# Kernel optimization log

Hardware: AMD Instinct MI355X
Metric: run time of the kernel (lower is better)

Reference implementation:

```python
import jax, jax.numpy as jnp
import numpy as np

N_NODES = 100000
N_EDGES = 3200000
F_IN = 128
HID = 256
EMB = 128
N_GRAPHS = 2048
N_CLASSES = 2


def _glorot(key, fan_in, fan_out):
    scale = np.sqrt(2.0 / (fan_in + fan_out)).astype(np.float32)
    return jax.random.normal(key, (fan_in, fan_out), jnp.float32) * scale


def setup_inputs() -> dict:
    key = jax.random.key(0)
    ks = jax.random.split(key, 12)
    x = jax.random.normal(ks[0], (N_NODES, F_IN), jnp.float32)
    edge_index = jax.random.randint(ks[1], (2, N_EDGES), 0, N_NODES, dtype=jnp.int64)
    batch = jnp.sort(jax.random.randint(ks[2], (N_NODES,), 0, N_GRAPHS, dtype=jnp.int64))
    return {
        "x": x,
        "edge_index": edge_index,
        "batch": batch,
        # GCN layer weights (input->hid, hid->hid, hid->emb)
        "W1": _glorot(ks[3], F_IN, HID), "b1": jnp.zeros((HID,), jnp.float32),
        "W2": _glorot(ks[4], HID, HID), "b2": jnp.zeros((HID,), jnp.float32),
        "W3": _glorot(ks[5], HID, EMB), "b3": jnp.zeros((EMB,), jnp.float32),
        # MLP classifier head
        "Wc1": _glorot(ks[6], EMB, HID), "bc1": jnp.zeros((HID,), jnp.float32),
        "Wc2": _glorot(ks[7], HID, HID // 2), "bc2": jnp.zeros((HID // 2,), jnp.float32),
        "Wc3": _glorot(ks[8], HID // 2, N_CLASSES), "bc3": jnp.zeros((N_CLASSES,), jnp.float32),
    }


def _gcn_conv(x, W, b, src, dst, dinv):
    # GCNConv with self loops: out = D^{-1/2}(A+I)D^{-1/2} (x @ W) + b
    h = x @ W  # [N, out]
    norm_e = dinv[src] * dinv[dst]  # [E]
    msg = h[src] * norm_e[:, None]
    agg = jax.ops.segment_sum(msg, dst, num_segments=N_NODES)
    agg = agg + h * (dinv * dinv)[:, None]  # self-loop term
    return agg + b


def reference(x, edge_index, batch, W1, b1, W2, b2, W3, b3, Wc1, bc1, Wc2, bc2, Wc3, bc3):
    src, dst = edge_index[0], edge_index[1]
    # degree including self loop (shared across layers)
    deg = jax.ops.segment_sum(jnp.ones((N_EDGES,), x.dtype), dst, num_segments=N_NODES) + 1.0
    dinv = jax.lax.rsqrt(deg)

    h = jax.nn.relu(_gcn_conv(x, W1, b1, src, dst, dinv))
    h = jax.nn.relu(_gcn_conv(h, W2, b2, src, dst, dinv))
    h = _gcn_conv(h, W3, b3, src, dst, dinv)  # final layer: no activation

    # mean pooling per graph
    sums = jax.ops.segment_sum(h, batch, num_segments=N_GRAPHS)  # [G, EMB]
    counts = jax.ops.segment_sum(jnp.ones((N_NODES,), h.dtype), batch, num_segments=N_GRAPHS)
    pooled = sums / jnp.maximum(counts, 1.0)[:, None]

    # MLP head (dropout is identity at eval)
    z = jax.nn.relu(pooled @ Wc1 + bc1)
    z = jax.nn.relu(z @ Wc2 + bc2)
    logits = z @ Wc3 + bc3  # [G, num_classes]
    return logits
```

## Files before the change

### kernel.cpp

```cpp
#include <hip/hip_runtime.h>
#include <cstdint>
#include <cstddef>

#define NODES  100000
#define EDGES  3200000
#define FIN    128
#define HIDDEN 256
#define EMBD   128
#define GRAPHS 2048

#define NB   256
#define NPB  391
#define CAP  16384
#define TILE 4096

typedef _Float16 f16;
typedef f16 f16x2 __attribute__((ext_vector_type(2)));
typedef f16 f16x4 __attribute__((ext_vector_type(4)));
typedef f16 f16x8 __attribute__((ext_vector_type(8)));
typedef float f32x4 __attribute__((ext_vector_type(4)));
typedef unsigned int u32;

__global__ __launch_bounds__(256) void binA_k(const int* __restrict__ src,
                                              const int* __restrict__ dst,
                                              u32* __restrict__ staging,
                                              int* __restrict__ gcur) {
  __shared__ u32 buf[TILE];
  __shared__ int bcnt[NB], bsh[NB], bstart[NB], bcur[NB], gbase[NB];
  const int tid = threadIdx.x;
  const int tb = blockIdx.x * TILE;

  bcnt[tid] = 0;
  __syncthreads();

#pragma unroll
  for (int j = 0; j < TILE / 256; ++j) {
    int i = tb + j * 256 + tid;
    if (i < EDGES) atomicAdd(&bcnt[dst[i] / NPB], 1);
  }
  __syncthreads();

  bsh[tid] = bcnt[tid];
  __syncthreads();
  for (int off = 1; off < NB; off <<= 1) {
    int t = (tid >= off) ? bsh[tid - off] : 0;
    __syncthreads();
    bsh[tid] += t;
    __syncthreads();
  }
  bstart[tid] = bsh[tid] - bcnt[tid];
  bcur[tid] = bsh[tid] - bcnt[tid];
  __syncthreads();

#pragma unroll
  for (int j = 0; j < TILE / 256; ++j) {
    int i = tb + j * 256 + tid;
    if (i < EDGES) {
      int d = dst[i];
      int b = d / NPB;
      u32 w = ((u32)src[i] << 9) | (u32)(d - b * NPB);
      buf[atomicAdd(&bcur[b], 1)] = w;
    }
  }
  gbase[tid] = atomicAdd(&gcur[tid], bcnt[tid]);
  __syncthreads();

  {
    int c = bcnt[tid], st = bstart[tid];
    u32* outp = staging + (size_t)tid * CAP + gbase[tid];
    for (int k = 0; k < c; ++k) outp[k] = buf[st + k];
  }
}

__global__ void bscan_k(const int* __restrict__ gcur, int* __restrict__ bbase) {
  __shared__ int sh[NB];
  int tid = threadIdx.x;
  int v = gcur[tid];
  sh[tid] = v;
  __syncthreads();
  for (int off = 1; off < NB; off <<= 1) {
    int t = (tid >= off) ? sh[tid - off] : 0;
    __syncthreads();
    sh[tid] += t;
    __syncthreads();
  }
  bbase[tid] = sh[tid] - v;
}

__global__ __launch_bounds__(512) void binB_k(const u32* __restrict__ staging,
                                              const int* __restrict__ gcur,
                                              const int* __restrict__ bbase,
                                              int* __restrict__ row_ptr,
                                              float* __restrict__ dinv,
                                              int* __restrict__ csr_src) {
  __shared__ int ncnt[512];
  __shared__ int ncur[512];
  const int b = blockIdx.x;
  const int tid = threadIdx.x;
  const int m = gcur[b];
  const int base = bbase[b];
  const int nb0 = b * NPB;
  const int nn = min(NPB, NODES - nb0);
  const u32* sb = staging + (size_t)b * CAP;

  ncnt[tid] = 0;
  __syncthreads();

  for (int k = tid; k < m; k += 512) atomicAdd(&ncnt[sb[k] & 511], 1);
  __syncthreads();

  int v = ncnt[tid];
  for (int off = 1; off < 512; off <<= 1) {
    int t = (tid >= off) ? ncnt[tid - off] : 0;
    __syncthreads();
    ncnt[tid] += t;
    __syncthreads();
  }
  int incl = ncnt[tid];
  if (tid < nn) {
    row_ptr[nb0 + tid + 1] = base + incl;
    dinv[nb0 + tid] = rsqrtf((float)(v + 1));
    ncur[tid] = base + incl - v;
  }
  if (b == 0 && tid == 0) row_ptr[0] = 0;
  __syncthreads();

  for (int k = tid; k < m; k += 512) {
    u32 w = sb[k];
    int pos = atomicAdd(&ncur[w & 511], 1);
    csr_src[pos] = (int)(w >> 9);
  }
}

__global__ void prescale_k(const float* __restrict__ x, const float* __restrict__ dinv,
                           f16* __restrict__ xs) {
  int idx = blockIdx.x * blockDim.x + threadIdx.x;
  if (idx >= NODES * FIN / 4) return;
  int row = idx >> 5;
  float4 v = *(const float4*)(x + (size_t)idx * 4);
  float d = dinv[row];
  f16x4 o = {(f16)(d * v.x), (f16)(d * v.y), (f16)(d * v.z), (f16)(d * v.w)};
  *(f16x4*)(xs + (size_t)idx * 4) = o;
}

__global__ void convw3_k(const float* __restrict__ W1, const float* __restrict__ W2,
                         const float* __restrict__ W3, f16* __restrict__ Wt1,
                         f16* __restrict__ Wt2, f16* __restrict__ Wt3) {
  int i = blockIdx.x * blockDim.x + threadIdx.x;
  if (i < 32768) {
    int k = i >> 8, m = i & 255;
    Wt1[(size_t)m * FIN + k] = (f16)W1[i];
  } else if (i < 98304) {
    int j = i - 32768;
    int k = j >> 8, m = j & 255;
    Wt2[(size_t)m * HIDDEN + k] = (f16)W2[j];
  } else if (i < 131072) {
    int j = i - 98304;
    int k = j >> 7, m = j & 127;
    Wt3[(size_t)m * HIDDEN + k] = (f16)W3[j];
  }
}

template <int V, bool FINAL>
__global__ __launch_bounds__(256) void agg_h(const f16* __restrict__ in, void* __restrict__ outv,
                      const int* __restrict__ row_ptr, const int* __restrict__ csr_src,
                      const float* __restrict__ dinv, const float* __restrict__ bias) {
  constexpr int D = V * 32;
  constexpr int U = 8;
  const int wid = (blockIdx.x * blockDim.x + threadIdx.x) >> 6;
  const int half = (threadIdx.x >> 5) & 1;
  const int lane = threadIdx.x & 31;
  const int node = wid * 2 + half;
  if (node >= NODES) return;
  const int c0 = lane * V;
  const f16* __restrict__ inc = in + c0;

  float acc[V];
#pragma unroll
  for (int v = 0; v < V; ++v) acc[v] = 0.f;

  const int beg = row_ptr[node], end = row_ptr[node + 1];
  int k = beg;
  if constexpr (V == 8) {
    for (; k + U <= end; k += U) {
      int s[U];
#pragma unroll
      for (int u = 0; u < U; ++u) s[u] = csr_src[k + u];
      f16x8 hv[U];
#pragma unroll
      for (int u = 0; u < U; ++u) hv[u] = *(const f16x8*)(inc + (size_t)s[u] * D);
#pragma unroll
      for (int u = 0; u < U; ++u)
#pragma unroll
        for (int v = 0; v < V; ++v) acc[v] += (float)hv[u][v];
    }
    for (; k < end; ++k) {
      f16x8 hv = *(const f16x8*)(inc + (size_t)csr_src[k] * D);
#pragma unroll
      for (int v = 0; v < V; ++v) acc[v] += (float)hv[v];
    }
    f16x8 hv = *(const f16x8*)(inc + (size_t)node * D);
#pragma unroll
    for (int v = 0; v < V; ++v) acc[v] += (float)hv[v];
  } else {
    for (; k + U <= end; k += U) {
      int s[U];
#pragma unroll
      for (int u = 0; u < U; ++u) s[u] = csr_src[k + u];
      f16x4 hv[U];
#pragma unroll
      for (int u = 0; u < U; ++u) hv[u] = *(const f16x4*)(inc + (size_t)s[u] * D);
#pragma unroll
      for (int u = 0; u < U; ++u)
#pragma unroll
        for (int v = 0; v < V; ++v) acc[v] += (float)hv[u][v];
    }
    for (; k < end; ++k) {
      f16x4 hv = *(const f16x4*)(inc + (size_t)csr_src[k] * D);
#pragma unroll
      for (int v = 0; v < V; ++v) acc[v] += (float)hv[v];
    }
    f16x4 hv = *(const f16x4*)(inc + (size_t)node * D);
#pragma unroll
    for (int v = 0; v < V; ++v) acc[v] += (float)hv[v];
  }

  const float di = dinv[node];
  if constexpr (FINAL) {
    float* out = (float*)outv;
    float4 o = {di * acc[0] + bias[c0], di * acc[1] + bias[c0 + 1],
                di * acc[2] + bias[c0 + 2], di * acc[3] + bias[c0 + 3]};
    *(float4*)(out + (size_t)node * D + c0) = o;
  } else {
    f16* out = (f16*)outv;
    if constexpr (V == 8) {
      f16x8 o;
#pragma unroll
      for (int v = 0; v < V; ++v) o[v] = (f16)(di * acc[v]);
      *(f16x8*)(out + (size_t)node * D + c0) = o;
    } else {
      f16x4 o;
#pragma unroll
      for (int v = 0; v < V; ++v) o[v] = (f16)(di * acc[v]);
      *(f16x4*)(out + (size_t)node * D + c0) = o;
    }
  }
}

template <int K>
__global__ __launch_bounds__(256, 2) void gemm_w(const f16* __restrict__ A,
                                                 const f16* __restrict__ Wt,
                                                 const float* __restrict__ bias,
                                                 const float* __restrict__ dinv,
                                                 f16* __restrict__ C, int N) {
  constexpr int M = 256;
  __shared__ f16 As[128][40];
  __shared__ f16 Bs[256][40];

  const int tid = threadIdx.x;
  const int rowbase = blockIdx.x * 128;
  const int l = tid & 63;
  const int wv = tid >> 6;
  const int wr = (wv >> 1) * 64;
  const int wc = (wv & 1) * 128;
  const int lr = tid >> 1;
  const int lc = (tid & 1) * 16;

  f32x4 acc[4][8];
#pragma unroll
  for (int i = 0; i < 4; ++i)
#pragma unroll
    for (int j = 0; j < 8; ++j) acc[i][j] = (f32x4){0.f, 0.f, 0.f, 0.f};

  const int arow = min(rowbase + lr, N - 1);
  const f16* aptr = A + (size_t)arow * K + lc;
  const f16* bptr = Wt + (size_t)tid * K;

  for (int kb = 0; kb < K; kb += 32) {
    *(f16x8*)&As[lr][lc]     = *(const f16x8*)(aptr + kb);
    *(f16x8*)&As[lr][lc + 8] = *(const f16x8*)(aptr + kb + 8);
#pragma unroll
    for (int q = 0; q < 4; ++q)
      *(f16x8*)&Bs[tid][q * 8] = *(const f16x8*)(bptr + kb + q * 8);
    __syncthreads();

    f16x8 a[4], b[8];
#pragma unroll
    for (int f = 0; f < 4; ++f)
      a[f] = *(const f16x8*)&As[wr + f * 16 + (l & 15)][(l >> 4) * 8];
#pragma unroll
    for (int g = 0; g < 8; ++g)
      b[g] = *(const f16x8*)&Bs[wc + g * 16 + (l & 15)][(l >> 4) * 8];
#pragma unroll
    for (int fm = 0; fm < 4; ++fm)
#pragma unroll
      for (int g = 0; g < 8; ++g)
        acc[fm][g] = __builtin_amdgcn_mfma_f32_16x16x32_f16(a[fm], b[g], acc[fm][g], 0, 0, 0);
    __syncthreads();
  }

  float bv[8];
#pragma unroll
  for (int g = 0; g < 8; ++g) bv[g] = bias[wc + g * 16 + (l & 15)];

#pragma unroll
  for (int fm = 0; fm < 4; ++fm) {
#pragma unroll
    for (int r = 0; r < 4; ++r) {
      int row = rowbase + wr + fm * 16 + (l >> 4) * 4 + r;
      if (row >= N) continue;
      float dv = dinv[row];
#pragma unroll
      for (int g = 0; g < 8; ++g) {
        int col = wc + g * 16 + (l & 15);
        float v = fmaxf(acc[fm][g][r] + bv[g], 0.f);
        C[(size_t)row * M + col] = (f16)(v * dv);
      }
    }
  }
}

template <int K, bool RELU, bool BIAS, bool DSCALE>
__global__ __launch_bounds__(256) void gemm_h(const f16* __restrict__ A,
                                              const f16* __restrict__ Wt,
                                              const float* __restrict__ bias,
                                              const float* __restrict__ dinv,
                                              f16* __restrict__ C, int N, int M) {
  __shared__ f16 As[128][40];
  __shared__ f16 Bs[128][40];

  const int tid = threadIdx.x;
  const int rowbase = blockIdx.x * 128;
  const int colbase = blockIdx.y * 128;
  const int l = tid & 63;
  const int wr = ((tid >> 6) >> 1) * 64;
  const int wc = ((tid >> 6) & 1) * 64;
  const int lr = tid >> 1;
  const int lc = (tid & 1) * 16;

  f32x4 acc[4][4];
#pragma unroll
  for (int i = 0; i < 4; ++i)
#pragma unroll
    for (int j = 0; j < 4; ++j) acc[i][j] = (f32x4){0.f, 0.f, 0.f, 0.f};

  const int arow = min(rowbase + lr, N - 1);
  const f16* aptr = A + (size_t)arow * K + lc;
  const f16* bptr = Wt + (size_t)(colbase + lr) * K + lc;

  for (int kb = 0; kb < K; kb += 32) {
    *(f16x8*)&As[lr][lc]     = *(const f16x8*)(aptr + kb);
    *(f16x8*)&As[lr][lc + 8] = *(const f16x8*)(aptr + kb + 8);
    *(f16x8*)&Bs[lr][lc]     = *(const f16x8*)(bptr + kb);
    *(f16x8*)&Bs[lr][lc + 8] = *(const f16x8*)(bptr + kb + 8);
    __syncthreads();

    f16x8 a[4], b[4];
#pragma unroll
    for (int f = 0; f < 4; ++f) {
      a[f] = *(const f16x8*)&As[wr + f * 16 + (l & 15)][(l >> 4) * 8];
      b[f] = *(const f16x8*)&Bs[wc + f * 16 + (l & 15)][(l >> 4) * 8];
    }
#pragma unroll
    for (int fm = 0; fm < 4; ++fm)
#pragma unroll
      for (int fn = 0; fn < 4; ++fn)
        acc[fm][fn] = __builtin_amdgcn_mfma_f32_16x16x32_f16(a[fm], b[fn], acc[fm][fn], 0, 0, 0);
    __syncthreads();
  }

  float bv[4];
#pragma unroll
  for (int fn = 0; fn < 4; ++fn)
    bv[fn] = BIAS ? bias[colbase + wc + fn * 16 + (l & 15)] : 0.f;

#pragma unroll
  for (int fm = 0; fm < 4; ++fm) {
#pragma unroll
    for (int r = 0; r < 4; ++r) {
      int row = rowbase + wr + fm * 16 + (l >> 4) * 4 + r;
      if (row >= N) continue;
      float dv = DSCALE ? dinv[row] : 1.f;
#pragma unroll
      for (int fn = 0; fn < 4; ++fn) {
        int col = colbase + wc + fn * 16 + (l & 15);
        float v = acc[fm][fn][r] + bv[fn];
        if (RELU) v = fmaxf(v, 0.f);
        C[(size_t)row * M + col] = (f16)(v * dv);
      }
    }
  }
}

template <int K, bool RELU, bool HAS_BIAS>
__global__ __launch_bounds__(256) void gemm_k(const float* __restrict__ A,
                                              const float* __restrict__ W,
                                              const float* __restrict__ bias,
                                              float* __restrict__ C, int N, int M) {
  constexpr int KB = 16;
  __shared__ float As[KB][128];
  __shared__ float Ws[KB][128];

  const int tid = threadIdx.x;
  const int rowbase = blockIdx.x * 128;
  const int colbase = blockIdx.y * 128;
  const int tr = tid >> 4;
  const int tc = tid & 15;
  const int ar = tid >> 1;
  const int ac4_0 = (tid & 1) * 2;
  const int wk = tid >> 4;
  const int wc4_0 = (tid & 15) * 2;

  float acc[8][8];
#pragma unroll
  for (int i = 0; i < 8; ++i)
#pragma unroll
    for (int j = 0; j < 8; ++j) acc[i][j] = 0.f;

  for (int kb = 0; kb < K; kb += KB) {
#pragma unroll
    for (int q = 0; q < 2; ++q) {
      int c4 = ac4_0 + q;
      int grow = rowbase + ar;
      float4 v = make_float4(0.f, 0.f, 0.f, 0.f);
      if (grow < N) v = *(const float4*)(A + (size_t)grow * K + kb + c4 * 4);
      As[c4 * 4 + 0][ar] = v.x;
      As[c4 * 4 + 1][ar] = v.y;
      As[c4 * 4 + 2][ar] = v.z;
      As[c4 * 4 + 3][ar] = v.w;
    }
#pragma unroll
    for (int q = 0; q < 2; ++q) {
      int c4 = wc4_0 + q;
      float4 v = *(const float4*)(W + (size_t)(kb + wk) * M + colbase + c4 * 4);
      *(float4*)&Ws[wk][c4 * 4] = v;
    }
    __syncthreads();

#pragma unroll
    for (int kk = 0; kk < KB; ++kk) {
      float4 a0 = *(const float4*)&As[kk][tr * 4];
      float4 a1 = *(const float4*)&As[kk][tr * 4 + 64];
      float4 w0 = *(const float4*)&Ws[kk][tc * 4];
      float4 w1 = *(const float4*)&Ws[kk][tc * 4 + 64];
      float a[8] = {a0.x, a0.y, a0.z, a0.w, a1.x, a1.y, a1.z, a1.w};
      float w[8] = {w0.x, w0.y, w0.z, w0.w, w1.x, w1.y, w1.z, w1.w};
#pragma unroll
      for (int i = 0; i < 8; ++i)
#pragma unroll
        for (int j = 0; j < 8; ++j) acc[i][j] = fmaf(a[i], w[j], acc[i][j]);
    }
    __syncthreads();
  }

#pragma unroll
  for (int i = 0; i < 8; ++i) {
    int r = rowbase + ((i < 4) ? (tr * 4 + i) : (64 + tr * 4 + (i - 4)));
    if (r >= N) continue;
#pragma unroll
    for (int jh = 0; jh < 2; ++jh) {
      int c = colbase + tc * 4 + jh * 64;
      float4 o;
      o.x = acc[i][jh * 4 + 0];
      o.y = acc[i][jh * 4 + 1];
      o.z = acc[i][jh * 4 + 2];
      o.w = acc[i][jh * 4 + 3];
      if (HAS_BIAS) {
        o.x += bias[c]; o.y += bias[c + 1]; o.z += bias[c + 2]; o.w += bias[c + 3];
      }
      if (RELU) {
        o.x = fmaxf(o.x, 0.f); o.y = fmaxf(o.y, 0.f);
        o.z = fmaxf(o.z, 0.f); o.w = fmaxf(o.w, 0.f);
      }
      *(float4*)(C + (size_t)r * M + c) = o;
    }
  }
}

__global__ void pool_k(const float* __restrict__ h, const int* __restrict__ batch,
                       float* __restrict__ pooled) {
  int g = blockIdx.x;
  int j = threadIdx.x;
  int lo = 0, hi = NODES;
  while (lo < hi) { int mid = (lo + hi) >> 1; if (batch[mid] < g) lo = mid + 1; else hi = mid; }
  int start = lo;
  int lo2 = start, hi2 = NODES;
  while (lo2 < hi2) { int mid = (lo2 + hi2) >> 1; if (batch[mid] < g + 1) lo2 = mid + 1; else hi2 = mid; }
  int end = lo2;
  float s = 0.f;
  for (int r = start; r < end; ++r) s += h[(size_t)r * EMBD + j];
  float c = (float)(end - start);
  pooled[g * EMBD + j] = s / fmaxf(c, 1.f);
}

__global__ void head_k(const float* __restrict__ z2, const float* __restrict__ Wc3,
                       const float* __restrict__ bc3, float* __restrict__ out) {
  int wv = (blockIdx.x * blockDim.x + threadIdx.x) >> 6;
  int lane = threadIdx.x & 63;
  if (wv >= GRAPHS) return;
  float2 z = *(const float2*)(z2 + (size_t)wv * 128 + lane * 2);
  int j0 = lane * 2;
  float a0 = z.x * Wc3[j0 * 2 + 0] + z.y * Wc3[(j0 + 1) * 2 + 0];
  float a1 = z.x * Wc3[j0 * 2 + 1] + z.y * Wc3[(j0 + 1) * 2 + 1];
  for (int off = 32; off; off >>= 1) {
    a0 += __shfl_down(a0, off);
    a1 += __shfl_down(a1, off);
  }
  if (lane == 0) {
    out[wv * 2 + 0] = a0 + bc3[0];
    out[wv * 2 + 1] = a1 + bc3[1];
  }
}

extern "C" void kernel_launch(void* const* d_in, const int* in_sizes, int n_in,
                              void* d_out, int out_size, void* d_ws, size_t ws_size,
                              hipStream_t stream) {
  const float* x    = (const float*)d_in[0];
  const int*   ei   = (const int*)d_in[1];
  const int*   batch= (const int*)d_in[2];
  const float* W1 = (const float*)d_in[3];  const float* b1 = (const float*)d_in[4];
  const float* W2 = (const float*)d_in[5];  const float* b2 = (const float*)d_in[6];
  const float* W3 = (const float*)d_in[7];  const float* b3 = (const float*)d_in[8];
  const float* Wc1= (const float*)d_in[9];  const float* bc1= (const float*)d_in[10];
  const float* Wc2= (const float*)d_in[11]; const float* bc2= (const float*)d_in[12];
  const float* Wc3= (const float*)d_in[13]; const float* bc3= (const float*)d_in[14];
  float* out = (float*)d_out;

  char* ws = (char*)d_ws;
  size_t off = 0;
  auto alloc = [&](size_t bytes) -> void* {
    void* p = ws + off;
    off = (off + bytes + 255) & ~(size_t)255;
    return p;
  };
  f16*   F0      = (f16*)alloc((size_t)NODES * 256 * 2);
  f16*   F1      = (f16*)alloc((size_t)NODES * 256 * 2);
  float* R0      = (float*)alloc((size_t)NODES * 128 * 4);
  int*   csr_src = (int*)alloc((size_t)EDGES * 4);
  u32*   staging = (u32*)alloc((size_t)NB * CAP * 4);
  int*   row_ptr = (int*)alloc((size_t)(NODES + 1) * 4);
  float* dinv    = (float*)alloc((size_t)NODES * 4);
  int*   gcur    = (int*)alloc(NB * 4);
  int*   bbase   = (int*)alloc(NB * 4);
  f16*   Wt1     = (f16*)alloc((size_t)FIN * HIDDEN * 2);
  f16*   Wt2     = (f16*)alloc((size_t)HIDDEN * HIDDEN * 2);
  f16*   Wt3     = (f16*)alloc((size_t)HIDDEN * EMBD * 2);
  float* pooled = (float*)F0;
  float* z1     = pooled + (size_t)GRAPHS * EMBD;
  float* z2     = z1 + (size_t)GRAPHS * HIDDEN;

  const int* srcA = ei;
  const int* dstA = ei + EDGES;

  hipMemsetAsync(gcur, 0, NB * 4, stream);
  binA_k<<<(EDGES + TILE - 1) / TILE, 256, 0, stream>>>(srcA, dstA, staging, gcur);
  bscan_k<<<1, NB, 0, stream>>>(gcur, bbase);
  binB_k<<<NB, 512, 0, stream>>>(staging, gcur, bbase, row_ptr, dinv, csr_src);

  convw3_k<<<(131072 + 255) / 256, 256, 0, stream>>>(W1, W2, W3, Wt1, Wt2, Wt3);
  prescale_k<<<(NODES * FIN / 4 + 255) / 256, 256, 0, stream>>>(x, dinv, F0);

  const int aggBlocks = ((NODES + 1) / 2 * 64 + 255) / 256;
  const int gemmRows = (NODES + 127) / 128;

  agg_h<4, false><<<aggBlocks, 256, 0, stream>>>(F0, F1, row_ptr, csr_src, dinv, nullptr);
  gemm_w<FIN><<<gemmRows, 256, 0, stream>>>(F1, Wt1, b1, dinv, F0, NODES);
  agg_h<8, false><<<aggBlocks, 256, 0, stream>>>(F0, F1, row_ptr, csr_src, dinv, nullptr);
  gemm_w<HIDDEN><<<gemmRows, 256, 0, stream>>>(F1, Wt2, b2, dinv, F0, NODES);
  gemm_h<HIDDEN, false, false, false><<<dim3(gemmRows, 1), 256, 0, stream>>>(F0, Wt3, nullptr, nullptr, F1, NODES, EMBD);
  agg_h<4, true><<<aggBlocks, 256, 0, stream>>>(F1, R0, row_ptr, csr_src, dinv, b3);

  pool_k<<<GRAPHS, 128, 0, stream>>>(R0, batch, pooled);
  gemm_k<EMBD, true, true><<<dim3((GRAPHS + 127) / 128, 2), 256, 0, stream>>>(pooled, Wc1, bc1, z1, GRAPHS, HIDDEN);
  gemm_k<HIDDEN, true, true><<<dim3((GRAPHS + 127) / 128, 1), 256, 0, stream>>>(z1, Wc2, bc2, z2, GRAPHS, EMBD);
  head_k<<<GRAPHS / 4, 256, 0, stream>>>(z2, Wc3, bc3, out);
}
```

Baseline: 705.5 us.

## Fuse layer-1 aggregation with GEMM, fold prescale into binning, fp16 final output

Adds a fused_l1 kernel that aggregates neighbours into a shared-memory tile and runs the layer-1 MFMA GEMM on it, so the aggregated intermediate never goes to global memory. The x prescale by dinv moves into binB_k, which removes one kernel launch and the global dinv reread. The final layer output and the pooling input become fp16 to halve that traffic, and the binning tile size doubles. The risks are lower occupancy in the fused kernel, because the gather and the GEMM share a block with a 128-row tile and a sync between them, and reduced precision for the final embeddings.

```diff
diff --git a/kernel.cpp b/kernel.cpp
--- a/kernel.cpp
+++ b/kernel.cpp
@@ -12,7 +12,7 @@
 #define NB   256
 #define NPB  391
 #define CAP  16384
-#define TILE 4096
+#define TILE 8192
 
 typedef _Float16 f16;
 typedef f16 f16x2 __attribute__((ext_vector_type(2)));
@@ -92,9 +92,12 @@
                                               const int* __restrict__ bbase,
                                               int* __restrict__ row_ptr,
                                               float* __restrict__ dinv,
-                                              int* __restrict__ csr_src) {
+                                              int* __restrict__ csr_src,
+                                              const float* __restrict__ x,
+                                              f16* __restrict__ xs) {
   __shared__ int ncnt[512];
   __shared__ int ncur[512];
+  __shared__ float sdinv[512];
   const int b = blockIdx.x;
   const int tid = threadIdx.x;
   const int m = gcur[b];
@@ -117,9 +120,11 @@
     __syncthreads();
   }
   int incl = ncnt[tid];
+  float dv = rsqrtf((float)(v + 1));
   if (tid < nn) {
     row_ptr[nb0 + tid + 1] = base + incl;
-    dinv[nb0 + tid] = rsqrtf((float)(v + 1));
+    dinv[nb0 + tid] = dv;
+    sdinv[tid] = dv;
     ncur[tid] = base + incl - v;
   }
   if (b == 0 && tid == 0) row_ptr[0] = 0;
@@ -130,17 +135,15 @@
     int pos = atomicAdd(&ncur[w & 511], 1);
     csr_src[pos] = (int)(w >> 9);
   }
-}
-
-__global__ void prescale_k(const float* __restrict__ x, const float* __restrict__ dinv,
-                           f16* __restrict__ xs) {
-  int idx = blockIdx.x * blockDim.x + threadIdx.x;
-  if (idx >= NODES * FIN / 4) return;
-  int row = idx >> 5;
-  float4 v = *(const float4*)(x + (size_t)idx * 4);
-  float d = dinv[row];
-  f16x4 o = {(f16)(d * v.x), (f16)(d * v.y), (f16)(d * v.z), (f16)(d * v.w)};
-  *(f16x4*)(xs + (size_t)idx * 4) = o;
+
+  for (int idx = tid; idx < nn * 32; idx += 512) {
+    int row = idx >> 5;
+    int c4 = idx & 31;
+    float d = sdinv[row];
+    float4 vx = *(const float4*)(x + (size_t)(nb0 + row) * FIN + c4 * 4);
+    f16x4 o = {(f16)(d * vx.x), (f16)(d * vx.y), (f16)(d * vx.z), (f16)(d * vx.w)};
+    *(f16x4*)(xs + (size_t)(nb0 + row) * FIN + c4 * 4) = o;
+  }
 }
 
 __global__ void convw3_k(const float* __restrict__ W1, const float* __restrict__ W2,
@@ -161,8 +164,95 @@
   }
 }
 
+__global__ __launch_bounds__(512, 4) void fused_l1(const f16* __restrict__ A,
+                                                   const f16* __restrict__ Wt1,
+                                                   const float* __restrict__ b1,
+                                                   const int* __restrict__ row_ptr,
+                                                   const int* __restrict__ csr_src,
+                                                   const float* __restrict__ dinv,
+                                                   f16* __restrict__ C) {
+  __shared__ f16 As[128][136];
+  const int tid = threadIdx.x;
+  const int rowbase = blockIdx.x * 128;
+  const int w = tid >> 6;
+  const int l = tid & 63;
+  const int half = (tid >> 5) & 1;
+  const int lane = tid & 31;
+  const int c0 = lane * 4;
+
+  const f16* __restrict__ inc = A + c0;
+  for (int p = 0; p < 8; ++p) {
+    const int lr = w * 16 + p * 2 + half;
+    const int node = rowbase + lr;
+    if (node < NODES) {
+      float acc[4] = {0.f, 0.f, 0.f, 0.f};
+      const int beg = row_ptr[node], end = row_ptr[node + 1];
+      int k = beg;
+      for (; k + 8 <= end; k += 8) {
+        int s[8];
+#pragma unroll
+        for (int u = 0; u < 8; ++u) s[u] = csr_src[k + u];
+        f16x4 hv[8];
+#pragma unroll
+        for (int u = 0; u < 8; ++u) hv[u] = *(const f16x4*)(inc + (size_t)s[u] * FIN);
+#pragma unroll
+        for (int u = 0; u < 8; ++u)
+#pragma unroll
+          for (int v = 0; v < 4; ++v) acc[v] += (float)hv[u][v];
+      }
+      for (; k < end; ++k) {
+        f16x4 hv = *(const f16x4*)(inc + (size_t)csr_src[k] * FIN);
+#pragma unroll
+        for (int v = 0; v < 4; ++v) acc[v] += (float)hv[v];
+      }
+      {
+        f16x4 hv = *(const f16x4*)(inc + (size_t)node * FIN);
+#pragma unroll
+        for (int v = 0; v < 4; ++v) acc[v] += (float)hv[v];
+      }
+      float di = dinv[node];
+      f16x4 o = {(f16)(di * acc[0]), (f16)(di * acc[1]),
+                 (f16)(di * acc[2]), (f16)(di * acc[3])};
+      *(f16x4*)&As[lr][c0] = o;
+    }
+  }
+  __syncthreads();
+
+  const int fr = l & 15;
+  const int kq = l >> 4;
+#pragma unroll
+  for (int ch = 0; ch < 2; ++ch) {
+    f32x4 acc[8];
+#pragma unroll
+    for (int cf = 0; cf < 8; ++cf) acc[cf] = (f32x4){0.f, 0.f, 0.f, 0.f};
+#pragma unroll
+    for (int kk = 0; kk < 4; ++kk) {
+      f16x8 a = *(const f16x8*)&As[w * 16 + fr][kk * 32 + kq * 8];
+#pragma unroll
+      for (int cf = 0; cf < 8; ++cf) {
+        int col = ch * 128 + cf * 16 + fr;
+        f16x8 b = *(const f16x8*)(Wt1 + (size_t)col * FIN + kk * 32 + kq * 8);
+        acc[cf] = __builtin_amdgcn_mfma_f32_16x16x32_f16(a, b, acc[cf], 0, 0, 0);
+      }
+    }
+#pragma unroll
+    for (int cf = 0; cf < 8; ++cf) {
+      int col = ch * 128 + cf * 16 + fr;
+      float bv = b1[col];
+#pragma unroll
+      for (int r = 0; r < 4; ++r) {
+        int row = rowbase + w * 16 + kq * 4 + r;
+        if (row < NODES) {
+          float v = fmaxf(acc[cf][r] + bv, 0.f) * dinv[row];
+          C[(size_t)row * HIDDEN + col] = (f16)v;
+        }
+      }
+    }
+  }
+}
+
 template <int V, bool FINAL>
-__global__ __launch_bounds__(256) void agg_h(const f16* __restrict__ in, void* __restrict__ outv,
+__global__ __launch_bounds__(256) void agg_h(const f16* __restrict__ in, f16* __restrict__ out,
                       const int* __restrict__ row_ptr, const int* __restrict__ csr_src,
                       const float* __restrict__ dinv, const float* __restrict__ bias) {
   constexpr int D = V * 32;
@@ -227,12 +317,11 @@
 
   const float di = dinv[node];
   if constexpr (FINAL) {
-    float* out = (float*)outv;
-    float4 o = {di * acc[0] + bias[c0], di * acc[1] + bias[c0 + 1],
-                di * acc[2] + bias[c0 + 2], di * acc[3] + bias[c0 + 3]};
-    *(float4*)(out + (size_t)node * D + c0) = o;
+    f16x4 o;
+#pragma unroll
+    for (int v = 0; v < V; ++v) o[v] = (f16)(di * acc[v] + bias[c0 + v]);
+    *(f16x4*)(out + (size_t)node * D + c0) = o;
   } else {
-    f16* out = (f16*)outv;
     if constexpr (V == 8) {
       f16x8 o;
 #pragma unroll
@@ -477,7 +566,7 @@
   }
 }
 
-__global__ void pool_k(const float* __restrict__ h, const int* __restrict__ batch,
+__global__ void pool_k(const f16* __restrict__ h, const int* __restrict__ batch,
                        float* __restrict__ pooled) {
   int g = blockIdx.x;
   int j = threadIdx.x;
@@ -488,7 +577,7 @@
   while (lo2 < hi2) { int mid = (lo2 + hi2) >> 1; if (batch[mid] < g + 1) lo2 = mid + 1; else hi2 = mid; }
   int end = lo2;
   float s = 0.f;
-  for (int r = start; r < end; ++r) s += h[(size_t)r * EMBD + j];
+  for (int r = start; r < end; ++r) s += (float)h[(size_t)r * EMBD + j];
   float c = (float)(end - start);
   pooled[g * EMBD + j] = s / fmaxf(c, 1.f);
 }
@@ -535,7 +624,7 @@
   };
   f16*   F0      = (f16*)alloc((size_t)NODES * 256 * 2);
   f16*   F1      = (f16*)alloc((size_t)NODES * 256 * 2);
-  float* R0      = (float*)alloc((size_t)NODES * 128 * 4);
+  f16*   hbuf    = (f16*)alloc((size_t)NODES * 128 * 2);
   int*   csr_src = (int*)alloc((size_t)EDGES * 4);
   u32*   staging = (u32*)alloc((size_t)NB * CAP * 4);
   int*   row_ptr = (int*)alloc((size_t)(NODES + 1) * 4);
@@ -545,7 +634,7 @@
   f16*   Wt1     = (f16*)alloc((size_t)FIN * HIDDEN * 2);
   f16*   Wt2     = (f16*)alloc((size_t)HIDDEN * HIDDEN * 2);
   f16*   Wt3     = (f16*)alloc((size_t)HIDDEN * EMBD * 2);
-  float* pooled = (float*)F0;
+  float* pooled = (float*)F1;
   float* z1     = pooled + (size_t)GRAPHS * EMBD;
   float* z2     = z1 + (size_t)GRAPHS * HIDDEN;
 
@@ -555,22 +644,20 @@
   hipMemsetAsync(gcur, 0, NB * 4, stream);
   binA_k<<<(EDGES + TILE - 1) / TILE, 256, 0, stream>>>(srcA, dstA, staging, gcur);
   bscan_k<<<1, NB, 0, stream>>>(gcur, bbase);
-  binB_k<<<NB, 512, 0, stream>>>(staging, gcur, bbase, row_ptr, dinv, csr_src);
+  binB_k<<<NB, 512, 0, stream>>>(staging, gcur, bbase, row_ptr, dinv, csr_src, x, F0);
 
   convw3_k<<<(131072 + 255) / 256, 256, 0, stream>>>(W1, W2, W3, Wt1, Wt2, Wt3);
-  prescale_k<<<(NODES * FIN / 4 + 255) / 256, 256, 0, stream>>>(x, dinv, F0);
 
   const int aggBlocks = ((NODES + 1) / 2 * 64 + 255) / 256;
   const int gemmRows = (NODES + 127) / 128;
 
-  agg_h<4, false><<<aggBlocks, 256, 0, stream>>>(F0, F1, row_ptr, csr_src, dinv, nullptr);
-  gemm_w<FIN><<<gemmRows, 256, 0, stream>>>(F1, Wt1, b1, dinv, F0, NODES);
-  agg_h<8, false><<<aggBlocks, 256, 0, stream>>>(F0, F1, row_ptr, csr_src, dinv, nullptr);
-  gemm_w<HIDDEN><<<gemmRows, 256, 0, stream>>>(F1, Wt2, b2, dinv, F0, NODES);
-  gemm_h<HIDDEN, false, false, false><<<dim3(gemmRows, 1), 256, 0, stream>>>(F0, Wt3, nullptr, nullptr, F1, NODES, EMBD);
-  agg_h<4, true><<<aggBlocks, 256, 0, stream>>>(F1, R0, row_ptr, csr_src, dinv, b3);
-
-  pool_k<<<GRAPHS, 128, 0, stream>>>(R0, batch, pooled);
+  fused_l1<<<gemmRows, 512, 0, stream>>>(F0, Wt1, b1, row_ptr, csr_src, dinv, F1);
+  agg_h<8, false><<<aggBlocks, 256, 0, stream>>>(F1, F0, row_ptr, csr_src, dinv, nullptr);
+  gemm_w<HIDDEN><<<gemmRows, 256, 0, stream>>>(F0, Wt2, b2, dinv, F1, NODES);
+  gemm_h<HIDDEN, false, false, false><<<dim3(gemmRows, 1), 256, 0, stream>>>(F1, Wt3, nullptr, nullptr, F0, NODES, EMBD);
+  agg_h<4, true><<<aggBlocks, 256, 0, stream>>>(F0, hbuf, row_ptr, csr_src, dinv, b3);
+
+  pool_k<<<GRAPHS, 128, 0, stream>>>(hbuf, batch, pooled);
   gemm_k<EMBD, true, true><<<dim3((GRAPHS + 127) / 128, 2), 256, 0, stream>>>(pooled, Wc1, bc1, z1, GRAPHS, HIDDEN);
   gemm_k<HIDDEN, true, true><<<dim3((GRAPHS + 127) / 128, 1), 256, 0, stream>>>(z1, Wc2, bc2, z2, GRAPHS, EMBD);
   head_k<<<GRAPHS / 4, 256, 0, stream>>>(z2, Wc3, bc3, out);
```

Result: slower. 774.3 us (+9.8%).
